# Kernel optimization log

Measured on AMD Instinct MI355X. Metric: run time of the kernel, lower is better.

Reference implementation:

```python
import jax, jax.numpy as jnp
import numpy as np
import math

INPUT_DIM = 16
R2 = math.sqrt(2.0)            # 1/sqrt(2) scaling on 2nd-order term
RD = math.sqrt(INPUT_DIM)      # sqrt(d)
RRD = math.sqrt(RD)            # d**0.25


def setup_inputs() -> dict:
    key = jax.random.key(0)
    x = jax.random.normal(key, (4, 16, 4096, INPUT_DIM), dtype=jnp.float32)
    return {"x": x}


def reference(x) -> jnp.ndarray:
    # x: (b, h, s, d)
    b, h, s, d = x.shape
    # 2nd-order term: outer product x_i * x_j flattened to d*d, / sqrt(2)
    x2 = jnp.einsum('bhsd,bhse->bhsde', x, x).reshape(b, h, s, d * d) / R2
    ones = jnp.ones_like(x[..., :1])  # x[..., :1] ** 0
    # concat along head_dim: [1, x/rrd, x2/rd] -> (b, h, s, 1 + d + d^2)
    return jnp.concatenate([ones, x / RRD, x2 / RD], axis=-1)
```

## Files before the change

### kernel.cpp

```cpp
#include <hip/hip_runtime.h>

#define INPUT_DIM 16
#define COLS 273
#define ROWS_PER_BLOCK 16
#define FLOATS_PER_BLOCK (ROWS_PER_BLOCK * COLS)
#define VEC4_PER_BLOCK (FLOATS_PER_BLOCK / 4)

#define S1 0.5f
#define S2 0.17677669529663687f

__global__ __launch_bounds__(256)
void taylor_exp_kernel(const float* __restrict__ x, float* __restrict__ out)
{
    __shared__ float xs[ROWS_PER_BLOCK * INPUT_DIM];

    const int tid = threadIdx.x;
    const long long rowBase = (long long)blockIdx.x * ROWS_PER_BLOCK;

    xs[tid] = x[rowBase * INPUT_DIM + tid];
    __syncthreads();

    float4* __restrict__ out4 =
        (float4*)(out + rowBase * COLS);

    #pragma unroll 1
    for (int v = tid; v < VEC4_PER_BLOCK; v += 256) {
        float vals[4];
        #pragma unroll
        for (int k = 0; k < 4; ++k) {
            const int g  = 4 * v + k;
            const int rl = g / COLS;
            const int c  = g - rl * COLS;
            const float* xr = &xs[rl * INPUT_DIM];
            float val;
            if (c == 0) {
                val = 1.0f;
            } else if (c <= INPUT_DIM) {
                val = xr[c - 1] * S1;
            } else {
                const int t = c - (INPUT_DIM + 1);
                val = xr[t >> 4] * xr[t & 15] * S2;
            }
            vals[k] = val;
        }
        float4 r;
        r.x = vals[0]; r.y = vals[1]; r.z = vals[2]; r.w = vals[3];
        out4[v] = r;
    }
}

extern "C" void kernel_launch(void* const* d_in, const int* in_sizes, int n_in,
                              void* d_out, int out_size, void* d_ws, size_t ws_size,
                              hipStream_t stream)
{
    const float* x = (const float*)d_in[0];
    float* out = (float*)d_out;

    const int nrows  = in_sizes[0] / INPUT_DIM;
    const int blocks = nrows / ROWS_PER_BLOCK;

    taylor_exp_kernel<<<blocks, 256, 0, stream>>>(x, out);
}
```

Before: 294.3 us.

## Stage output tile in LDS and compute outer product per thread without divides

Each thread now computes one column of the outer product for its row, using float4 reads of the row from shared memory, and writes the results into a shared-memory output tile. After a barrier, the tile is copied to global memory with coalesced float4 stores. This removes the per-element integer division, modulo and branching of the old index-driven loop. In exchange it uses about 17KB of LDS per block, which may lower occupancy, and adds a second barrier.

```diff
diff --git a/kernel.cpp b/kernel.cpp
--- a/kernel.cpp
+++ b/kernel.cpp
@@ -13,6 +13,7 @@
 void taylor_exp_kernel(const float* __restrict__ x, float* __restrict__ out)
 {
     __shared__ float xs[ROWS_PER_BLOCK * INPUT_DIM];
+    __shared__ float os[FLOATS_PER_BLOCK];
 
     const int tid = threadIdx.x;
     const long long rowBase = (long long)blockIdx.x * ROWS_PER_BLOCK;
@@ -20,32 +21,48 @@
     xs[tid] = x[rowBase * INPUT_DIM + tid];
     __syncthreads();
 
-    float4* __restrict__ out4 =
-        (float4*)(out + rowBase * COLS);
+    const int row = tid >> 4;
+    const int l   = tid & 15;
+    const int base = row * COLS;
 
-    #pragma unroll 1
-    for (int v = tid; v < VEC4_PER_BLOCK; v += 256) {
-        float vals[4];
-        #pragma unroll
-        for (int k = 0; k < 4; ++k) {
-            const int g  = 4 * v + k;
-            const int rl = g / COLS;
-            const int c  = g - rl * COLS;
-            const float* xr = &xs[rl * INPUT_DIM];
-            float val;
-            if (c == 0) {
-                val = 1.0f;
-            } else if (c <= INPUT_DIM) {
-                val = xr[c - 1] * S1;
-            } else {
-                const int t = c - (INPUT_DIM + 1);
-                val = xr[t >> 4] * xr[t & 15] * S2;
-            }
-            vals[k] = val;
+    const float xl = xs[tid];
+
+    const float4* xsr = (const float4*)&xs[row * INPUT_DIM];
+    const float4 r0 = xsr[0], r1 = xsr[1], r2 = xsr[2], r3 = xsr[3];
+
+    os[base + 1 + l] = xl * S1;
+    if (l == 0) os[base] = 1.0f;
+
+    const float p = xl * S2;
+    float* o2 = &os[base + 17 + l];
+    o2[ 0 * 16] = r0.x * p;
+    o2[ 1 * 16] = r0.y * p;
+    o2[ 2 * 16] = r0.z * p;
+    o2[ 3 * 16] = r0.w * p;
+    o2[ 4 * 16] = r1.x * p;
+    o2[ 5 * 16] = r1.y * p;
+    o2[ 6 * 16] = r1.z * p;
+    o2[ 7 * 16] = r1.w * p;
+    o2[ 8 * 16] = r2.x * p;
+    o2[ 9 * 16] = r2.y * p;
+    o2[10 * 16] = r2.z * p;
+    o2[11 * 16] = r2.w * p;
+    o2[12 * 16] = r3.x * p;
+    o2[13 * 16] = r3.y * p;
+    o2[14 * 16] = r3.z * p;
+    o2[15 * 16] = r3.w * p;
+
+    __syncthreads();
+
+    float4* __restrict__ out4 = (float4*)(out + (long long)blockIdx.x * FLOATS_PER_BLOCK);
+    const float4* os4 = (const float4*)os;
+
+    #pragma unroll
+    for (int it = 0; it < 5; ++it) {
+        const int v = tid + it * 256;
+        if (v < VEC4_PER_BLOCK) {
+            out4[v] = os4[v];
         }
-        float4 r;
-        r.x = vals[0]; r.y = vals[1]; r.z = vals[2]; r.w = vals[3];
-        out4[v] = r;
     }
 }
 
```

After: 297.4 us. About the same (+1.0%).
